# Performance work log

Hardware: AMD Instinct MI355X
Metric: run time of the kernel (lower is better)

The kernel has to match this reference:

```python
import jax, jax.numpy as jnp
import numpy as np

B = 8192          # batch_size
NB = 4096         # num_banks (== mask length)
PAD = NB // 2     # reflect pad on each side


def setup_inputs() -> dict:
    key = jax.random.key(0)
    k1, k2, k3 = jax.random.split(key, 3)
    logits = jax.random.normal(k1, (NB,), dtype=jnp.float32) * 0.1
    u = jax.random.uniform(k2, (B, NB), dtype=jnp.float32)          # Bernoulli uniforms
    shift = jax.random.randint(k3, (B,), 0, NB, dtype=jnp.int32)    # per-sample shift
    return {"logits": logits, "u": u, "shift": shift}


def reference(logits, u, shift):
    # Bernoulli(sigmoid(logits)) sample via inverse-CDF on externally supplied uniforms
    p = jax.nn.sigmoid(logits)                       # (NB,)
    grid = (u < p).astype(jnp.float32)               # (B, NB)
    # Bernoulli log_prob summed over banks: g*log(p) + (1-g)*log(1-p)
    log_probs = (grid * jax.nn.log_sigmoid(logits)
                 + (1.0 - grid) * jax.nn.log_sigmoid(-logits)).sum(axis=1)  # (B,)
    # reflect-pad along bank axis, then gather a shifted window of length NB
    padded = jnp.pad(grid, ((0, 0), (PAD, PAD)), mode="reflect")    # (B, NB+2*PAD)
    idx = shift[:, None].astype(jnp.int32) + jnp.arange(NB, dtype=jnp.int32)[None, :]
    masks = jnp.take_along_axis(padded, idx, axis=1)[:, None, :]    # (B, 1, NB)
    return masks, log_probs
```

## Files before the change

### kernel.cpp

```cpp
#include <hip/hip_runtime.h>
#include <math.h>

#define NB 4096
#define PAD 2048
#define BLOCK 256

__device__ __forceinline__ int mirror_idx(int i) {
    i = ::abs(i);
    return (i < NB) ? i : (2 * (NB - 1) - i);
}

__global__ void fbmp_precompute(const float* __restrict__ logits, float* __restrict__ ws) {
    int j = blockIdx.x * blockDim.x + threadIdx.x;
    if (j >= NB) return;
    float x = logits[j];
    double xd = (double)x;
    float e = (float)exp(-xd);
    float p = 1.0f / (1.0f + e);
    float lsp = (float)(-log1p(exp(-xd)));
    float lsn = (float)(-log1p(exp(xd)));
    ws[j] = p;
    ws[NB + j] = lsp;
    ws[2 * NB + j] = lsn;
}

__global__ __launch_bounds__(BLOCK) void fbmp_main(
    const float* __restrict__ u, const int* __restrict__ shift,
    const float* __restrict__ ws,
    float* __restrict__ masks, float* __restrict__ logp)
{
    __shared__ float sg[NB];
    __shared__ float sred[BLOCK / 64];

    const int b = blockIdx.x;
    const float4* __restrict__ u4   = (const float4*)(u + (size_t)b * NB);
    const float4* __restrict__ p4   = (const float4*)(ws);
    const float4* __restrict__ lsp4 = (const float4*)(ws + NB);
    const float4* __restrict__ lsn4 = (const float4*)(ws + 2 * NB);

    float acc = 0.0f;
    for (int i = threadIdx.x; i < NB / 4; i += BLOCK) {
        float4 uv = u4[i];
        float4 pv = p4[i];
        float4 ap = lsp4[i];
        float4 an = lsn4[i];
        bool c0 = uv.x < pv.x;
        bool c1 = uv.y < pv.y;
        bool c2 = uv.z < pv.z;
        bool c3 = uv.w < pv.w;
        acc += (c0 ? ap.x : an.x) + (c1 ? ap.y : an.y)
             + (c2 ? ap.z : an.z) + (c3 ? ap.w : an.w);
        float4 g;
        g.x = c0 ? 1.0f : 0.0f;
        g.y = c1 ? 1.0f : 0.0f;
        g.z = c2 ? 1.0f : 0.0f;
        g.w = c3 ? 1.0f : 0.0f;
        ((float4*)sg)[i] = g;
    }

    #pragma unroll
    for (int off = 32; off > 0; off >>= 1)
        acc += __shfl_down(acc, off, 64);
    const int lane = threadIdx.x & 63;
    const int wid  = threadIdx.x >> 6;
    if (lane == 0) sred[wid] = acc;
    __syncthreads();
    if (threadIdx.x == 0) {
        float t = 0.0f;
        #pragma unroll
        for (int w = 0; w < BLOCK / 64; ++w) t += sred[w];
        logp[b] = t;
    }

    const int s = shift[b] - PAD;
    float4* __restrict__ m4 = (float4*)(masks + (size_t)b * NB);
    for (int i = threadIdx.x; i < NB / 4; i += BLOCK) {
        int k = 4 * i + s;
        float4 o;
        o.x = sg[mirror_idx(k + 0)];
        o.y = sg[mirror_idx(k + 1)];
        o.z = sg[mirror_idx(k + 2)];
        o.w = sg[mirror_idx(k + 3)];
        m4[i] = o;
    }
}

extern "C" void kernel_launch(void* const* d_in, const int* in_sizes, int n_in,
                              void* d_out, int out_size, void* d_ws, size_t ws_size,
                              hipStream_t stream) {
    const float* logits = (const float*)d_in[0];
    const float* u      = (const float*)d_in[1];
    const int*   shift  = (const int*)d_in[2];
    const int B = in_sizes[2];

    float* ws    = (float*)d_ws;
    float* masks = (float*)d_out;
    float* logp  = (float*)d_out + (size_t)B * NB;

    fbmp_precompute<<<(NB + 255) / 256, 256, 0, stream>>>(logits, ws);
    fbmp_main<<<B, BLOCK, 0, stream>>>(u, shift, ws, masks, logp);
}
```

Baseline: 241.9 us.

## Software-prefetch inputs, use scalar nontemporal mask stores, raise occupancy hint

Unrolls the sampling loop into a register double-buffered software pipeline that loads the next chunk of u and the precomputed tables while the current chunk is processed. Moves the shift load earlier and adds a min-blocks-per-CU launch bound. The mask write becomes scalar per-thread stores with nontemporal hints instead of float4 stores, which makes shared-memory reads contiguous per lane. The kernel is a memory-bound streaming kernel, so the scalar global stores may cost more store instructions than they save.

```diff
diff --git a/kernel.cpp b/kernel.cpp
--- a/kernel.cpp
+++ b/kernel.cpp
@@ -4,6 +4,7 @@
 #define NB 4096
 #define PAD 2048
 #define BLOCK 256
+#define ITERS (NB / 4 / BLOCK)
 
 __device__ __forceinline__ int mirror_idx(int i) {
     i = ::abs(i);
@@ -24,7 +25,7 @@
     ws[2 * NB + j] = lsn;
 }
 
-__global__ __launch_bounds__(BLOCK) void fbmp_main(
+__global__ __launch_bounds__(BLOCK, 8) void fbmp_main(
     const float* __restrict__ u, const int* __restrict__ shift,
     const float* __restrict__ ws,
     float* __restrict__ masks, float* __restrict__ logp)
@@ -33,29 +34,45 @@
     __shared__ float sred[BLOCK / 64];
 
     const int b = blockIdx.x;
+    const int s = shift[b] - PAD;
+
     const float4* __restrict__ u4   = (const float4*)(u + (size_t)b * NB);
     const float4* __restrict__ p4   = (const float4*)(ws);
     const float4* __restrict__ lsp4 = (const float4*)(ws + NB);
     const float4* __restrict__ lsn4 = (const float4*)(ws + 2 * NB);
 
     float acc = 0.0f;
-    for (int i = threadIdx.x; i < NB / 4; i += BLOCK) {
-        float4 uv = u4[i];
-        float4 pv = p4[i];
-        float4 ap = lsp4[i];
-        float4 an = lsn4[i];
-        bool c0 = uv.x < pv.x;
-        bool c1 = uv.y < pv.y;
-        bool c2 = uv.z < pv.z;
-        bool c3 = uv.w < pv.w;
-        acc += (c0 ? ap.x : an.x) + (c1 ? ap.y : an.y)
-             + (c2 ? ap.z : an.z) + (c3 ? ap.w : an.w);
-        float4 g;
-        g.x = c0 ? 1.0f : 0.0f;
-        g.y = c1 ? 1.0f : 0.0f;
-        g.z = c2 ? 1.0f : 0.0f;
-        g.w = c3 ? 1.0f : 0.0f;
-        ((float4*)sg)[i] = g;
+    {
+        const int t = threadIdx.x;
+        float4 uv = u4[t];
+        float4 pv = p4[t];
+        float4 ap = lsp4[t];
+        float4 an = lsn4[t];
+        #pragma unroll
+        for (int it = 0; it < ITERS; ++it) {
+            float4 nuv, npv, nap, nan2;
+            if (it + 1 < ITERS) {
+                const int i1 = t + (it + 1) * BLOCK;
+                nuv = u4[i1];
+                npv = p4[i1];
+                nap = lsp4[i1];
+                nan2 = lsn4[i1];
+            }
+            const int i = t + it * BLOCK;
+            bool c0 = uv.x < pv.x;
+            bool c1 = uv.y < pv.y;
+            bool c2 = uv.z < pv.z;
+            bool c3 = uv.w < pv.w;
+            acc += (c0 ? ap.x : an.x) + (c1 ? ap.y : an.y)
+                 + (c2 ? ap.z : an.z) + (c3 ? ap.w : an.w);
+            float4 g;
+            g.x = c0 ? 1.0f : 0.0f;
+            g.y = c1 ? 1.0f : 0.0f;
+            g.z = c2 ? 1.0f : 0.0f;
+            g.w = c3 ? 1.0f : 0.0f;
+            ((float4*)sg)[i] = g;
+            uv = nuv; pv = npv; ap = nap; an = nan2;
+        }
     }
 
     #pragma unroll
@@ -72,16 +89,12 @@
         logp[b] = t;
     }
 
-    const int s = shift[b] - PAD;
-    float4* __restrict__ m4 = (float4*)(masks + (size_t)b * NB);
-    for (int i = threadIdx.x; i < NB / 4; i += BLOCK) {
-        int k = 4 * i + s;
-        float4 o;
-        o.x = sg[mirror_idx(k + 0)];
-        o.y = sg[mirror_idx(k + 1)];
-        o.z = sg[mirror_idx(k + 2)];
-        o.w = sg[mirror_idx(k + 3)];
-        m4[i] = o;
+    float* __restrict__ mrow = masks + (size_t)b * NB;
+    #pragma unroll
+    for (int it = 0; it < NB / BLOCK; ++it) {
+        const int k = threadIdx.x + it * BLOCK;
+        float v = sg[mirror_idx(k + s)];
+        __builtin_nontemporal_store(v, &mrow[k]);
     }
 }
 
```

Result: no change. 240.7 us (-0.5%).

## Split kernel into bit-packed grid pass and separate mask scatter pass

Applied to the files above, without the earlier changes.

Replaces the single fused kernel with two kernels. The first computes log-probs and packs each row's Bernoulli results into 64 ballot bitmasks in workspace. The second reads those bits into a small shared array and writes the reflected, shifted mask with nontemporal stores. The aim is a small shared-memory footprint for higher occupancy and streaming output writes. The cost is an extra launch, a workspace round trip, and heavier index arithmetic, with the old fused path kept as a fallback when the workspace is too small.

```diff
diff --git a/kernel.cpp b/kernel.cpp
--- a/kernel.cpp
+++ b/kernel.cpp
@@ -4,6 +4,9 @@
 #define NB 4096
 #define PAD 2048
 #define BLOCK 256
+#define QITERS (NB / 4 / BLOCK)
+
+typedef float f32x4 __attribute__((ext_vector_type(4)));
 
 __device__ __forceinline__ int mirror_idx(int i) {
     i = ::abs(i);
@@ -24,7 +27,105 @@
     ws[2 * NB + j] = lsn;
 }
 
-__global__ __launch_bounds__(BLOCK) void fbmp_main(
+__global__ __launch_bounds__(BLOCK, 8) void fbmp_grid(
+    const float* __restrict__ u, const float* __restrict__ ws,
+    unsigned long long* __restrict__ pb, float* __restrict__ logp)
+{
+    __shared__ float sred[BLOCK / 64];
+
+    const int b = blockIdx.x;
+    const int t = threadIdx.x;
+    const int lane = t & 63;
+    const int wid  = t >> 6;
+
+    const float4* __restrict__ u4   = (const float4*)(u + (size_t)b * NB);
+    const float4* __restrict__ p4   = (const float4*)(ws);
+    const float4* __restrict__ lsp4 = (const float4*)(ws + NB);
+    const float4* __restrict__ lsn4 = (const float4*)(ws + 2 * NB);
+    unsigned long long* __restrict__ pbrow = pb + (size_t)b * 64;
+
+    float acc = 0.0f;
+    #pragma unroll
+    for (int it = 0; it < QITERS; ++it) {
+        const int i = t + it * BLOCK;
+        float4 uv = u4[i];
+        float4 pv = p4[i];
+        float4 ap = lsp4[i];
+        float4 an = lsn4[i];
+        bool c0 = uv.x < pv.x;
+        bool c1 = uv.y < pv.y;
+        bool c2 = uv.z < pv.z;
+        bool c3 = uv.w < pv.w;
+        acc += (c0 ? ap.x : an.x) + (c1 ? ap.y : an.y)
+             + (c2 ? ap.z : an.z) + (c3 ? ap.w : an.w);
+        unsigned long long b0 = __ballot(c0);
+        unsigned long long b1 = __ballot(c1);
+        unsigned long long b2 = __ballot(c2);
+        unsigned long long b3 = __ballot(c3);
+        if (lane == 0) {
+            unsigned long long* __restrict__ w8 = pbrow + ((it * 4 + wid) << 2);
+            w8[0] = b0; w8[1] = b1; w8[2] = b2; w8[3] = b3;
+        }
+    }
+
+    #pragma unroll
+    for (int off = 32; off > 0; off >>= 1)
+        acc += __shfl_down(acc, off, 64);
+    if (lane == 0) sred[wid] = acc;
+    __syncthreads();
+    if (t == 0) {
+        float tt = 0.0f;
+        #pragma unroll
+        for (int w = 0; w < BLOCK / 64; ++w) tt += sred[w];
+        logp[b] = tt;
+    }
+}
+
+__global__ __launch_bounds__(BLOCK, 8) void fbmp_scatter(
+    const unsigned long long* __restrict__ pb, const int* __restrict__ shift,
+    float* __restrict__ masks)
+{
+    __shared__ unsigned int sw[128];
+
+    const int b = blockIdx.x;
+    const int t = threadIdx.x;
+    const int s = shift[b] - PAD;
+
+    const unsigned int* __restrict__ pbrow32 = (const unsigned int*)(pb + (size_t)b * 64);
+    if (t < 128) sw[t] = pbrow32[t];
+    __syncthreads();
+
+    float* __restrict__ mrow = masks + (size_t)b * NB;
+    #pragma unroll
+    for (int it = 0; it < QITERS; ++it) {
+        const int i = t + it * BLOCK;
+        const int k = 4 * i + s;
+        f32x4 o;
+        {
+            const int j = mirror_idx(k + 0);
+            const int widx = ((j >> 10) << 5) | (((j >> 8) & 3) << 3) | ((j & 3) << 1) | ((j >> 7) & 1);
+            o.x = ((sw[widx] >> ((j >> 2) & 31)) & 1u) ? 1.0f : 0.0f;
+        }
+        {
+            const int j = mirror_idx(k + 1);
+            const int widx = ((j >> 10) << 5) | (((j >> 8) & 3) << 3) | ((j & 3) << 1) | ((j >> 7) & 1);
+            o.y = ((sw[widx] >> ((j >> 2) & 31)) & 1u) ? 1.0f : 0.0f;
+        }
+        {
+            const int j = mirror_idx(k + 2);
+            const int widx = ((j >> 10) << 5) | (((j >> 8) & 3) << 3) | ((j & 3) << 1) | ((j >> 7) & 1);
+            o.z = ((sw[widx] >> ((j >> 2) & 31)) & 1u) ? 1.0f : 0.0f;
+        }
+        {
+            const int j = mirror_idx(k + 3);
+            const int widx = ((j >> 10) << 5) | (((j >> 8) & 3) << 3) | ((j & 3) << 1) | ((j >> 7) & 1);
+            o.w = ((sw[widx] >> ((j >> 2) & 31)) & 1u) ? 1.0f : 0.0f;
+        }
+        __builtin_nontemporal_store(o, (f32x4*)mrow + i);
+    }
+}
+
+__global__ __launch_bounds__(BLOCK) void fbmp_fused(
     const float* __restrict__ u, const int* __restrict__ shift,
     const float* __restrict__ ws,
     float* __restrict__ masks, float* __restrict__ logp)
@@ -57,7 +158,6 @@
         g.w = c3 ? 1.0f : 0.0f;
         ((float4*)sg)[i] = g;
     }
-
     #pragma unroll
     for (int off = 32; off > 0; off >>= 1)
         acc += __shfl_down(acc, off, 64);
@@ -71,7 +171,6 @@
         for (int w = 0; w < BLOCK / 64; ++w) t += sred[w];
         logp[b] = t;
     }
-
     const int s = shift[b] - PAD;
     float4* __restrict__ m4 = (float4*)(masks + (size_t)b * NB);
     for (int i = threadIdx.x; i < NB / 4; i += BLOCK) {
@@ -98,5 +197,14 @@
     float* logp  = (float*)d_out + (size_t)B * NB;
 
     fbmp_precompute<<<(NB + 255) / 256, 256, 0, stream>>>(logits, ws);
-    fbmp_main<<<B, BLOCK, 0, stream>>>(u, shift, ws, masks, logp);
-}
+
+    const size_t tbl_bytes = (size_t)3 * NB * sizeof(float);
+    const size_t pb_bytes  = (size_t)B * 64 * sizeof(unsigned long long);
+    if (ws_size >= tbl_bytes + pb_bytes) {
+        unsigned long long* pb = (unsigned long long*)((char*)d_ws + tbl_bytes);
+        fbmp_grid<<<B, BLOCK, 0, stream>>>(u, ws, pb, logp);
+        fbmp_scatter<<<B, BLOCK, 0, stream>>>(pb, shift, masks);
+    } else {
+        fbmp_fused<<<B, BLOCK, 0, stream>>>(u, shift, ws, masks, logp);
+    }
+}
```

Result: no change. 242.8 us (+0.4%).

## Split into bit-packed grid kernel and shifted-window scatter kernel

Applied to the files above, without the earlier changes.

Splits the fused kernel in two. The first processes 8 rows per block with register double-buffered loads of u and per-thread cached p/log tables, writing the Bernoulli grid as ballot bitmasks to workspace. The second reads the packed bits (512 B per row) and writes the reflect-padded shifted masks with nontemporal stores, 8 rows per block. This aims to cut shared-memory traffic and per-block overhead and improve load/store streaming, at the cost of an extra launch and a small workspace round trip. It falls back to the old fused kernel if the workspace is too small.

```diff
diff --git a/kernel.cpp b/kernel.cpp
--- a/kernel.cpp
+++ b/kernel.cpp
@@ -4,6 +4,11 @@
 #define NB 4096
 #define PAD 2048
 #define BLOCK 256
+#define QITERS (NB / 4 / BLOCK)
+#define ROWS_A 8
+#define ROWS_B 8
+
+typedef float f32x4 __attribute__((ext_vector_type(4)));
 
 __device__ __forceinline__ int mirror_idx(int i) {
     i = ::abs(i);
@@ -24,7 +29,147 @@
     ws[2 * NB + j] = lsn;
 }
 
-__global__ __launch_bounds__(BLOCK) void fbmp_main(
+#define GRID_ROW(R, CUR, NXT)                                                  \
+    if ((R) < nrows) {                                                         \
+        if ((R) + 1 < nrows) {                                                 \
+            const float4* __restrict__ nr4 =                                   \
+                (const float4*)(u + (size_t)(b0 + (R) + 1) * NB);              \
+            _Pragma("unroll")                                                  \
+            for (int c = 0; c < QITERS; ++c) NXT[c] = nr4[t + c * BLOCK];      \
+        }                                                                      \
+        float acc = 0.0f;                                                      \
+        unsigned int* __restrict__ pr = pb32 + (size_t)(b0 + (R)) * 128;       \
+        _Pragma("unroll")                                                      \
+        for (int c = 0; c < QITERS; ++c) {                                     \
+            bool c0 = CUR[c].x < Tp[c].x;                                      \
+            bool c1 = CUR[c].y < Tp[c].y;                                      \
+            bool c2 = CUR[c].z < Tp[c].z;                                      \
+            bool c3 = CUR[c].w < Tp[c].w;                                      \
+            acc += (c0 ? Tlp[c].x : Tln[c].x) + (c1 ? Tlp[c].y : Tln[c].y)     \
+                 + (c2 ? Tlp[c].z : Tln[c].z) + (c3 ? Tlp[c].w : Tln[c].w);    \
+            unsigned long long B0 = __ballot(c0), B1 = __ballot(c1);           \
+            unsigned long long B2 = __ballot(c2), B3 = __ballot(c3);           \
+            if (lane == 0) {                                                   \
+                uint4 lo = make_uint4((unsigned)B0, (unsigned)B1,              \
+                                      (unsigned)B2, (unsigned)B3);             \
+                uint4 hi = make_uint4((unsigned)(B0 >> 32), (unsigned)(B1 >> 32),\
+                                      (unsigned)(B2 >> 32), (unsigned)(B3 >> 32));\
+                uint4* __restrict__ dst = (uint4*)(pr + 32 * c + 8 * wid);     \
+                dst[0] = lo;                                                   \
+                dst[1] = hi;                                                   \
+            }                                                                  \
+        }                                                                      \
+        _Pragma("unroll")                                                      \
+        for (int off = 32; off > 0; off >>= 1)                                 \
+            acc += __shfl_down(acc, off, 64);                                  \
+        if (lane == 0) sredAll[(R)][wid] = acc;                                \
+    }
+
+__global__ __launch_bounds__(BLOCK, 4) void fbmp_grid(
+    const float* __restrict__ u, const float* __restrict__ ws,
+    unsigned int* __restrict__ pb32, float* __restrict__ logp, int B)
+{
+    __shared__ float sredAll[ROWS_A][BLOCK / 64];
+
+    const int t = threadIdx.x;
+    const int lane = t & 63;
+    const int wid  = t >> 6;
+    const int b0 = blockIdx.x * ROWS_A;
+    const int nrows = (B - b0 < ROWS_A) ? (B - b0) : ROWS_A;
+
+    const float4* __restrict__ p4   = (const float4*)(ws);
+    const float4* __restrict__ lsp4 = (const float4*)(ws + NB);
+    const float4* __restrict__ lsn4 = (const float4*)(ws + 2 * NB);
+
+    float4 Tp[QITERS], Tlp[QITERS], Tln[QITERS];
+    #pragma unroll
+    for (int c = 0; c < QITERS; ++c) {
+        Tp[c]  = p4[t + c * BLOCK];
+        Tlp[c] = lsp4[t + c * BLOCK];
+        Tln[c] = lsn4[t + c * BLOCK];
+    }
+
+    float4 bufA[QITERS], bufB[QITERS];
+    {
+        const float4* __restrict__ r4 = (const float4*)(u + (size_t)b0 * NB);
+        #pragma unroll
+        for (int c = 0; c < QITERS; ++c) bufA[c] = r4[t + c * BLOCK];
+    }
+
+    GRID_ROW(0, bufA, bufB)
+    GRID_ROW(1, bufB, bufA)
+    GRID_ROW(2, bufA, bufB)
+    GRID_ROW(3, bufB, bufA)
+    GRID_ROW(4, bufA, bufB)
+    GRID_ROW(5, bufB, bufA)
+    GRID_ROW(6, bufA, bufB)
+    GRID_ROW(7, bufB, bufA)
+
+    __syncthreads();
+    if (t < nrows) {
+        float tt = 0.0f;
+        #pragma unroll
+        for (int w = 0; w < BLOCK / 64; ++w) tt += sredAll[t][w];
+        logp[b0 + t] = tt;
+    }
+}
+
+__global__ __launch_bounds__(BLOCK, 8) void fbmp_scatter(
+    const unsigned int* __restrict__ pb32, const int* __restrict__ shift,
+    float* __restrict__ masks, int B)
+{
+    __shared__ unsigned int sw[2][128];
+
+    const int t = threadIdx.x;
+    const int b0 = blockIdx.x * ROWS_B;
+    const int nrows = (B - b0 < ROWS_B) ? (B - b0) : ROWS_B;
+
+    unsigned int wn = 0;
+    if (t < 128) wn = pb32[(size_t)b0 * 128 + t];
+    int scur = shift[b0] - PAD;
+    if (t < 128) sw[0][t] = wn;
+
+    for (int r = 0; r < nrows; ++r) {
+        const int buf = r & 1;
+        int snext = 0;
+        if (r + 1 < nrows) {
+            if (t < 128) wn = pb32[(size_t)(b0 + r + 1) * 128 + t];
+            snext = shift[b0 + r + 1] - PAD;
+        }
+        __syncthreads();
+
+        const unsigned int* __restrict__ sb = sw[buf];
+        float* __restrict__ mrow = masks + (size_t)(b0 + r) * NB;
+        #pragma unroll
+        for (int c = 0; c < QITERS; ++c) {
+            const int i = t + c * BLOCK;
+            const int k = 4 * i + scur;
+            f32x4 o;
+            {
+                const int j = mirror_idx(k + 0);
+                o.x = ((sb[((j >> 7) << 2) | (j & 3)] >> ((j >> 2) & 31)) & 1u) ? 1.0f : 0.0f;
+            }
+            {
+                const int j = mirror_idx(k + 1);
+                o.y = ((sb[((j >> 7) << 2) | (j & 3)] >> ((j >> 2) & 31)) & 1u) ? 1.0f : 0.0f;
+            }
+            {
+                const int j = mirror_idx(k + 2);
+                o.z = ((sb[((j >> 7) << 2) | (j & 3)] >> ((j >> 2) & 31)) & 1u) ? 1.0f : 0.0f;
+            }
+            {
+                const int j = mirror_idx(k + 3);
+                o.w = ((sb[((j >> 7) << 2) | (j & 3)] >> ((j >> 2) & 31)) & 1u) ? 1.0f : 0.0f;
+            }
+            __builtin_nontemporal_store(o, (f32x4*)mrow + i);
+        }
+
+        if (r + 1 < nrows && t < 128) sw[buf ^ 1][t] = wn;
+        scur = snext;
+    }
+}
+
+__global__ __launch_bounds__(BLOCK) void fbmp_fused(
     const float* __restrict__ u, const int* __restrict__ shift,
     const float* __restrict__ ws,
     float* __restrict__ masks, float* __restrict__ logp)
@@ -57,7 +202,6 @@
         g.w = c3 ? 1.0f : 0.0f;
         ((float4*)sg)[i] = g;
     }
-
     #pragma unroll
     for (int off = 32; off > 0; off >>= 1)
         acc += __shfl_down(acc, off, 64);
@@ -71,7 +215,6 @@
         for (int w = 0; w < BLOCK / 64; ++w) t += sred[w];
         logp[b] = t;
     }
-
     const int s = shift[b] - PAD;
     float4* __restrict__ m4 = (float4*)(masks + (size_t)b * NB);
     for (int i = threadIdx.x; i < NB / 4; i += BLOCK) {
@@ -98,5 +241,16 @@
     float* logp  = (float*)d_out + (size_t)B * NB;
 
     fbmp_precompute<<<(NB + 255) / 256, 256, 0, stream>>>(logits, ws);
-    fbmp_main<<<B, BLOCK, 0, stream>>>(u, shift, ws, masks, logp);
-}
+
+    const size_t tbl_bytes = (size_t)3 * NB * sizeof(float);
+    const size_t pb_bytes  = (size_t)B * 128 * sizeof(unsigned int);
+    if (ws_size >= tbl_bytes + pb_bytes) {
+        unsigned int* pb32 = (unsigned int*)((char*)d_ws + tbl_bytes);
+        const int gA = (B + ROWS_A - 1) / ROWS_A;
+        const int gB = (B + ROWS_B - 1) / ROWS_B;
+        fbmp_grid<<<gA, BLOCK, 0, stream>>>(u, ws, pb32, logp, B);
+        fbmp_scatter<<<gB, BLOCK, 0, stream>>>(pb32, shift, masks, B);
+    } else {
+        fbmp_fused<<<B, BLOCK, 0, stream>>>(u, shift, ws, masks, logp);
+    }
+}
```

Result: slower. 249.5 us (+3.1%).
